# Kernel tuning notes

Measured on AMD Instinct MI355X. Metric: run time of the kernel, lower is better.

## Reference

```python
import jax, jax.numpy as jnp
import numpy as np

N_HEADS = 4  # top-k experts per token (init arg n_heads)


def setup_inputs() -> dict:
    key = jax.random.key(0)
    k1, k2, k3, k4 = jax.random.split(key, 4)
    dmodel, n_experts, expert_size = 1024, 64, 128
    B, S = 4, 2048
    x = jax.random.normal(k1, (B, S, dmodel), dtype=jnp.float32)
    # init stds follow the module: sel ~ d^-0.5, keys ~ d^-0.5, values ~ (n_experts*expert_size)^-0.5
    expert_sel = jax.random.normal(k2, (n_experts, dmodel), dtype=jnp.float32) * (dmodel ** -0.5)
    keys = jax.random.normal(k3, (n_experts, dmodel, expert_size), dtype=jnp.float32) * (dmodel ** -0.5)
    values = jax.random.normal(k4, (n_experts, expert_size, dmodel), dtype=jnp.float32) * ((n_experts * expert_size) ** -0.5)
    return {"x": x, "expert_sel": expert_sel, "keys": keys, "values": values}


def reference(x, expert_sel, keys, values):
    B, S, d = x.shape
    n_experts = keys.shape[0]
    xf = x.reshape(-1, d)                               # [N, d]
    N = xf.shape[0]
    # expert selection: sigmoid gates, top-k experts per token
    logits = xf @ expert_sel.T                           # [N, K]
    sel = jax.nn.sigmoid(logits)
    sel_val, sel_idx = jax.lax.top_k(sel, N_HEADS)       # [N, H]
    # dense gate mask: gate[n,k] = sigmoid gate if expert k selected else 0
    gates = jnp.zeros((N, n_experts), dtype=x.dtype)
    gates = gates.at[jnp.arange(N)[:, None], sel_idx].set(sel_val)
    # per-expert key projection + ReLU + gate (relu(0)*0 == 0 so dense-masked form is exact)
    h = jnp.einsum('nd,kde->nke', xf, keys)              # [N, K, E]
    scores = jax.nn.relu(h) * gates[:, :, None]
    # weighted gather-sum over per-expert values (embedding_bag mode='sum')
    out = jnp.einsum('nke,kev->nv', scores, values)      # [N, v_dim]
    return out.reshape(B, S, -1)
```

## Files before the change

### kernel.cpp

```cpp
#include <hip/hip_runtime.h>

typedef __bf16 bf16x8 __attribute__((ext_vector_type(8)));
typedef float f32x4 __attribute__((ext_vector_type(4)));

#define N_TOK 8192
#define DMODEL 1024
#define NEXP 64
#define ESIZE 128
#define WL_MAX 576
#define PREP_SPLIT 2064

__device__ __forceinline__ unsigned short f2bf(float f) {
  unsigned int u = __builtin_bit_cast(unsigned int, f);
  u += 0x7FFFu + ((u >> 16) & 1u);
  return (unsigned short)(u >> 16);
}

__device__ __forceinline__ float b2f(unsigned short u) {
  unsigned int v = ((unsigned int)u) << 16;
  return __builtin_bit_cast(float, v);
}

__device__ __forceinline__ void gld16(unsigned short* lds, const unsigned short* g) {
  __builtin_amdgcn_global_load_lds(
      (const __attribute__((address_space(1))) unsigned int*)g,
      (__attribute__((address_space(3))) unsigned int*)lds, 16, 0, 0);
}

__global__ void k_prep(const float* __restrict__ x, unsigned short* __restrict__ xh,
                       unsigned short* __restrict__ xl, const float* __restrict__ esel,
                       unsigned short* __restrict__ sh_, unsigned short* __restrict__ sl_,
                       int* __restrict__ zeroPtr) {
  int bid = blockIdx.x, tid = threadIdx.x;
  if (bid == 0 && tid < 128) zeroPtr[tid] = 0;
  size_t gid = (size_t)bid * 256 + tid;
  const size_t NX = (size_t)N_TOK * DMODEL / 16;
  const float* in;
  unsigned short *ho, *lo2;
  size_t i;
  if (gid < NX) {
    in = x; ho = xh; lo2 = xl; i = gid * 16;
  } else {
    in = esel; ho = sh_; lo2 = sl_; i = (gid - NX) * 16;
  }
#pragma unroll
  for (int c = 0; c < 2; ++c) {
    size_t ii = i + c * 8;
    float4 a = *reinterpret_cast<const float4*>(in + ii);
    float4 b = *reinterpret_cast<const float4*>(in + ii + 4);
    unsigned short h[8], l[8];
    float v[8] = {a.x, a.y, a.z, a.w, b.x, b.y, b.z, b.w};
#pragma unroll
    for (int q = 0; q < 8; ++q) {
      h[q] = f2bf(v[q]);
      l[q] = f2bf(v[q] - b2f(h[q]));
    }
    uint4 oh, ol;
    oh.x = h[0] | ((unsigned)h[1] << 16); oh.y = h[2] | ((unsigned)h[3] << 16);
    oh.z = h[4] | ((unsigned)h[5] << 16); oh.w = h[6] | ((unsigned)h[7] << 16);
    ol.x = l[0] | ((unsigned)l[1] << 16); ol.y = l[2] | ((unsigned)l[3] << 16);
    ol.z = l[4] | ((unsigned)l[5] << 16); ol.w = l[6] | ((unsigned)l[7] << 16);
    *reinterpret_cast<uint4*>(ho + ii) = oh;
    *reinterpret_cast<uint4*>(lo2 + ii) = ol;
  }
}

__global__ __launch_bounds__(512) void k_rlogit(const unsigned short* __restrict__ xh,
                                                const unsigned short* __restrict__ xl,
                                                const unsigned short* __restrict__ sh,
                                                const unsigned short* __restrict__ sl,
                                                const float* __restrict__ keys,
                                                unsigned short* __restrict__ kout,
                                                const float* __restrict__ values,
                                                unsigned short* __restrict__ vout,
                                                int4* __restrict__ idx4,
                                                float4* __restrict__ g4,
                                                int* __restrict__ gcount,
                                                int* __restrict__ glist) {
  int tid = threadIdx.x, lane = tid & 63;

  __shared__ alignas(16) unsigned short stage[24576];

  if (blockIdx.x >= 256) {
    int tt = (blockIdx.x - 256) * 2 + (tid >> 8);
    int ts = tid & 255;
    float* tb = (float*)stage + (tid >> 8) * (64 * 65);
    const float* in;
    unsigned short* out;
    int R, C;
    if (tt < 2048) { in = keys; out = kout; R = DMODEL; C = ESIZE; }
    else { in = values; out = vout; R = ESIZE; C = DMODEL; tt -= 2048; }
    int b = tt >> 5, tile = tt & 31;
    int tilesC = C >> 6;
    int tr = tile / tilesC, tc = tile % tilesC;
    const float* ip = in + (size_t)b * R * C + (size_t)tr * 64 * C + tc * 64;
    unsigned short* op = out + (size_t)b * R * C + (size_t)tc * 64 * R + tr * 64;

    int lr = ts >> 4, lc4 = (ts & 15) * 4;
#pragma unroll
    for (int p = 0; p < 4; ++p) {
      int row = p * 16 + lr;
      *reinterpret_cast<float4*>(&tb[row * 65 + lc4]) =
          *reinterpret_cast<const float4*>(ip + (size_t)row * C + lc4);
    }
    __syncthreads();
    int orow = ts >> 3, oc = (ts & 7) * 8;
#pragma unroll
    for (int p = 0; p < 2; ++p) {
      int row = p * 32 + orow;
      unsigned short h[8];
#pragma unroll
      for (int j = 0; j < 8; ++j) h[j] = f2bf(tb[(oc + j) * 65 + row]);
      uint4 ov;
      ov.x = h[0] | ((unsigned)h[1] << 16); ov.y = h[2] | ((unsigned)h[3] << 16);
      ov.z = h[4] | ((unsigned)h[5] << 16); ov.w = h[6] | ((unsigned)h[7] << 16);
      *reinterpret_cast<uint4*>(op + (size_t)row * R + oc) = ov;
    }
    return;
  }

  int tok0 = blockIdx.x * 32;
  int wv = tid >> 6, wr = wv >> 2, wc = wv & 3;
  int cc = lane & 15, grp = lane >> 4;

  int aslot = tid & 255;
  int arow = aslot >> 3, ach = aslot & 7;
  const unsigned short* srcA = (tid < 256 ? xh : xl) +
      (size_t)(tok0 + arow) * DMODEL + ((ach ^ (arow & 7)) * 8);
  int brow = tid >> 3, bch = tid & 7;
  int bsw = (bch ^ (brow & 7)) * 8;
  const unsigned short* srcBh = sh + (size_t)brow * DMODEL + bsw;
  const unsigned short* srcBl = sl + (size_t)brow * DMODEL + bsw;

  auto stg = [&](int bo , int kk) {
    unsigned short* s = stage + bo;
    gld16(s + tid * 8, srcA + kk);
    gld16(s + 4096 + tid * 8, srcBh + kk);
    gld16(s + 8192 + tid * 8, srcBl + kk);
  };

  f32x4 acc = {};
  stg(0, 0);
  __syncthreads();
  const char* sb = (const char*)stage;
  int ra = wr * 16 + cc;
  int rb = wc * 16 + cc;
  for (int t = 0; t < 16; ++t) {
    int curB = (t & 1) * 24576;
    if (t < 15) stg(((t + 1) & 1) * 12288, (t + 1) * 64);
#pragma unroll
    for (int ks = 0; ks < 2; ++ks) {
      int o_a = (((ks * 4 + grp) ^ (ra & 7)) * 16);
      int o_b = (((ks * 4 + grp) ^ (rb & 7)) * 16);
      bf16x8 aH = *reinterpret_cast<const bf16x8*>(sb + curB + ra * 128 + o_a);
      bf16x8 aL = *reinterpret_cast<const bf16x8*>(sb + curB + 4096 + ra * 128 + o_a);
      bf16x8 bH = *reinterpret_cast<const bf16x8*>(sb + curB + 8192 + rb * 128 + o_b);
      bf16x8 bL = *reinterpret_cast<const bf16x8*>(sb + curB + 16384 + rb * 128 + o_b);
      acc = __builtin_amdgcn_mfma_f32_16x16x32_bf16(aH, bH, acc, 0, 0, 0);
      acc = __builtin_amdgcn_mfma_f32_16x16x32_bf16(aH, bL, acc, 0, 0, 0);
      acc = __builtin_amdgcn_mfma_f32_16x16x32_bf16(aL, bH, acc, 0, 0, 0);
    }
    __syncthreads();
  }

  float* lg = (float*)stage;
#pragma unroll
  for (int r = 0; r < 4; ++r)
    lg[(wr * 16 + grp * 4 + r) * 68 + wc * 16 + cc] = acc[r];
  __syncthreads();

  if (tid < 32) {
    float bv0 = -3e38f, bv1 = -3e38f, bv2 = -3e38f, bv3 = -3e38f, bv4 = -3e38f;
    int bi0 = 0, bi1 = 0, bi2 = 0, bi3 = 0;
    for (int e = 0; e < 64; ++e) {
      float v = lg[tid * 68 + e];
      if (v > bv4) {
        if (v > bv0) {
          bv4 = bv3; bv3 = bv2; bi3 = bi2; bv2 = bv1; bi2 = bi1; bv1 = bv0; bi1 = bi0; bv0 = v; bi0 = e;
        } else if (v > bv1) {
          bv4 = bv3; bv3 = bv2; bi3 = bi2; bv2 = bv1; bi2 = bi1; bv1 = v; bi1 = e;
        } else if (v > bv2) {
          bv4 = bv3; bv3 = bv2; bi3 = bi2; bv2 = v; bi2 = e;
        } else if (v > bv3) {
          bv4 = bv3; bv3 = v; bi3 = e;
        } else {
          bv4 = v;
        }
      }
    }
    idx4[tok0 + tid] = make_int4(bi0, bi1, bi2, bi3);
    float4 g;
    g.x = 1.0f / (1.0f + __expf(-bv0));
    g.y = 1.0f / (1.0f + __expf(-bv1));
    g.z = 1.0f / (1.0f + __expf(-bv2));
    g.w = 1.0f / (1.0f + __expf(-bv3));
    g4[tok0 + tid] = g;
    if (bv3 - bv4 < 1e-4f) {
      int p = atomicAdd(gcount, 1);
      glist[p] = tok0 + tid;
    }
  }
}

__global__ __launch_bounds__(256) void k_refine(const float* __restrict__ x,
                                                const float* __restrict__ esel,
                                                const int* __restrict__ gcount,
                                                const int* __restrict__ glist,
                                                int4* __restrict__ idx4,
                                                float4* __restrict__ g4) {
  __shared__ double lp[256];
  __shared__ double lgt[64];
  int cnt = *gcount;
  for (int i = blockIdx.x; i < cnt; i += 64) {
    int n = glist[i];
    int e = threadIdx.x & 63, jq = threadIdx.x >> 6;
    const float* xr = x + (size_t)n * DMODEL + jq * 256;
    const float* er = esel + (size_t)e * DMODEL + jq * 256;
    double s = 0.0;
    for (int j = 0; j < 256; ++j)
      s += (double)xr[j] * (double)er[j];
    lp[threadIdx.x] = s;
    __syncthreads();
    if (threadIdx.x < 64)
      lgt[threadIdx.x] =
          lp[threadIdx.x] + lp[64 + threadIdx.x] + lp[128 + threadIdx.x] + lp[192 + threadIdx.x];
    __syncthreads();
    if (threadIdx.x == 0) {
      double bv0 = -1.0e300, bv1 = -1.0e300, bv2 = -1.0e300, bv3 = -1.0e300;
      int bi0 = 0, bi1 = 0, bi2 = 0, bi3 = 0;
      for (int e2 = 0; e2 < 64; ++e2) {
        double v = lgt[e2];
        if (v > bv3) {
          if (v > bv0) {
            bv3 = bv2; bi3 = bi2; bv2 = bv1; bi2 = bi1; bv1 = bv0; bi1 = bi0; bv0 = v; bi0 = e2;
          } else if (v > bv1) {
            bv3 = bv2; bi3 = bi2; bv2 = bv1; bi2 = bi1; bv1 = v; bi1 = e2;
          } else if (v > bv2) {
            bv3 = bv2; bi3 = bi2; bv2 = v; bi2 = e2;
          } else {
            bv3 = v; bi3 = e2;
          }
        }
      }
      idx4[n] = make_int4(bi0, bi1, bi2, bi3);
      float4 g;
      g.x = 1.0f / (1.0f + __expf(-(float)bv0));
      g.y = 1.0f / (1.0f + __expf(-(float)bv1));
      g.z = 1.0f / (1.0f + __expf(-(float)bv2));
      g.w = 1.0f / (1.0f + __expf(-(float)bv3));
      g4[n] = g;
    }
    __syncthreads();
  }
}

__global__ __launch_bounds__(256) void k_bucket(const int4* __restrict__ idx4,
                                                const float4* __restrict__ g4,
                                                int* __restrict__ btok,
                                                float* __restrict__ bgate,
                                                int* __restrict__ cnt) {
  __shared__ int lcnt[64];
  __shared__ int lbase[64];
  int tid = threadIdx.x;
  if (tid < 64) lcnt[tid] = 0;
  __syncthreads();
  int n = blockIdx.x * 256 + tid;
  int4 I = idx4[n];
  float4 G = g4[n];
  int e[4] = {I.x, I.y, I.z, I.w};
  float g[4] = {G.x, G.y, G.z, G.w};
  int pos[4];
#pragma unroll
  for (int h = 0; h < 4; ++h) pos[h] = atomicAdd(&lcnt[e[h]], 1);
  __syncthreads();
  if (tid < 64 && lcnt[tid] > 0) lbase[tid] = atomicAdd(&cnt[tid], lcnt[tid]);
  __syncthreads();
#pragma unroll
  for (int h = 0; h < 4; ++h) {
    int slot = lbase[e[h]] + pos[h];
    btok[e[h] * N_TOK + slot] = h * N_TOK + n;
    bgate[e[h] * N_TOK + slot] = g[h];
  }
}

__global__ void k_worklist(const int* __restrict__ cnt, int* __restrict__ wl) {
  int lane = threadIdx.x;
  int nt = (cnt[lane] + 63) >> 6;
  int off = nt;
  for (int d = 1; d < 64; d <<= 1) {
    int o = __shfl_up(off, d);
    if (lane >= d) off += o;
  }
  int total = __shfl(off, 63);
  off -= nt;
  for (int t = 0; t < nt; ++t) wl[off + t] = (lane << 8) | t;
  for (int i = total + lane; i < WL_MAX; i += 64) wl[i] = -1;
}

__global__ __launch_bounds__(512, 6) void k_expert(
    const unsigned short* __restrict__ xbf, const unsigned short* __restrict__ kbf,
    const unsigned short* __restrict__ vbf, const int* __restrict__ wl,
    const int* __restrict__ btok, const float* __restrict__ bgate,
    const int* __restrict__ cnt, unsigned short* __restrict__ part) {
  int wid = (blockIdx.x & 7) * (WL_MAX / 8) + (blockIdx.x >> 3);
  int wle = wl[wid];
  if (wle < 0) return;
  int k = wle >> 8, tile = wle & 255;
  int ck = cnt[k];
  int tid = threadIdx.x, lane = tid & 63;
  int wv = tid >> 6, wr = wv >> 2, wc = wv & 3;
  int cc = lane & 15, grp = lane >> 4;

  __shared__ alignas(16) unsigned short stage[25088];
  __shared__ int sRow[64];
  __shared__ float sGate[64];

  if (tid < 64) {
    int i = tile * 64 + tid;
    bool valid = i < ck;
    sRow[tid] = valid ? btok[k * N_TOK + i] : 4 * N_TOK + wid;
    sGate[tid] = valid ? bgate[k * N_TOK + i] : 0.0f;
  }
  __syncthreads();

  const unsigned short* kb = kbf + (size_t)k * (ESIZE * DMODEL);
  const unsigned short* vb = vbf + (size_t)k * (DMODEL * ESIZE);
  char* sbase = (char*)stage;

  int arow = tid >> 3, ach = tid & 7;
  const unsigned short* srcA =
      xbf + (size_t)(sRow[arow] & (N_TOK - 1)) * DMODEL + ((ach ^ (arow & 7)) * 8);
  int b1row = 64 + arow;
  const unsigned short* srcB0 = kb + (size_t)arow * DMODEL + ((ach ^ (arow & 7)) * 8);
  const unsigned short* srcB1 = kb + (size_t)b1row * DMODEL + ((ach ^ (b1row & 7)) * 8);

  auto stg1 = [&](int boB, int kk) {
    unsigned short* s = (unsigned short*)(sbase + boB);
    gld16(s + tid * 8, srcA + kk);
    gld16(s + 4096 + tid * 8, srcB0 + kk);
    gld16(s + 8192 + tid * 8, srcB1 + kk);
  };

  f32x4 acc[2][2] = {};
  stg1(0, 0);
  __syncthreads();
  for (int t = 0; t < 16; ++t) {
    int curB = (t & 1) * 24576;
    if (t < 15) stg1(((t + 1) & 1) * 24576, (t + 1) * 64);
    bf16x8 aF[2][2], bF[2][2];
#pragma unroll
    for (int ks = 0; ks < 2; ++ks) {
#pragma unroll
      for (int m = 0; m < 2; ++m) {
        int r = wr * 32 + m * 16 + cc;
        aF[ks][m] = *reinterpret_cast<const bf16x8*>(
            sbase + curB + r * 128 + (((ks * 4 + grp) ^ (r & 7)) * 16));
      }
#pragma unroll
      for (int n = 0; n < 2; ++n) {
        int r = wc * 32 + n * 16 + cc;
        bF[ks][n] = *reinterpret_cast<const bf16x8*>(
            sbase + curB + 8192 + r * 128 + (((ks * 4 + grp) ^ (r & 7)) * 16));
      }
    }
#pragma unroll
    for (int ks = 0; ks < 2; ++ks)
#pragma unroll
      for (int m = 0; m < 2; ++m)
#pragma unroll
        for (int n = 0; n < 2; ++n)
          acc[m][n] = __builtin_amdgcn_mfma_f32_16x16x32_bf16(aF[ks][m], bF[ks][n], acc[m][n], 0, 0, 0);
    __syncthreads();
  }

  int v0row = tid >> 4, vch = tid & 15;
  int v1row = 32 + v0row;
  const unsigned short* srcV0 = vb + (size_t)v0row * ESIZE + ((vch ^ (v0row & 15)) * 8);
  const unsigned short* srcV1 = vb + (size_t)v1row * ESIZE + ((vch ^ (v1row & 15)) * 8);
  auto stgV = [&](int boB, int ch) {
    unsigned short* s = (unsigned short*)(sbase + boB);
    const size_t co = (size_t)ch * 64 * ESIZE;
    gld16(s + tid * 8, srcV0 + co);
    gld16(s + 4096 + tid * 8, srcV1 + co);
  };

  stgV(17408, 0);

#pragma unroll
  for (int m = 0; m < 2; ++m) {
    int trow = wr * 32 + m * 16 + grp * 4;
#pragma unroll
    for (int n = 0; n < 2; ++n) {
      int e = wc * 32 + n * 16 + cc;
#pragma unroll
      for (int r = 0; r < 4; ++r) {
        float s = acc[m][n][r];
        s = s > 0.0f ? s * sGate[trow + r] : 0.0f;
        stage[(trow + r) * 136 + e] = f2bf(s);
      }
    }
  }
  __syncthreads();

  bf16x8 sF[2][4];
#pragma unroll
  for (int m = 0; m < 2; ++m) {
    int r = wr * 32 + m * 16 + cc;
#pragma unroll
    for (int ks = 0; ks < 4; ++ks)
      sF[m][ks] = *reinterpret_cast<const bf16x8*>((const char*)stage + r * 272 + ks * 64 + grp * 16);
  }
  unsigned short* rB[2][4];
#pragma unroll
  for (int m = 0; m < 2; ++m)
#pragma unroll
    for (int r = 0; r < 4; ++r)
      rB[m][r] = part + (size_t)sRow[wr * 32 + m * 16 + grp * 4 + r] * DMODEL + wc * 16 + cc;

  for (int ch = 0; ch < 16; ++ch) {
    int curB = 17408 + (ch & 1) * 16384;
    if (ch < 15) stgV(17408 + (((ch + 1) & 1) * 16384), ch + 1);
    int r = wc * 16 + cc;
    bf16x8 vF[4];
#pragma unroll
    for (int ks = 0; ks < 4; ++ks)
      vF[ks] = *reinterpret_cast<const bf16x8*>(
          sbase + curB + r * 256 + (((ks * 4 + grp) ^ cc) * 16));
    f32x4 o[2] = {};
#pragma unroll
    for (int ks = 0; ks < 4; ++ks)
#pragma unroll
      for (int m = 0; m < 2; ++m)
        o[m] = __builtin_amdgcn_mfma_f32_16x16x32_bf16(sF[m][ks], vF[ks], o[m], 0, 0, 0);
#pragma unroll
    for (int m = 0; m < 2; ++m)
#pragma unroll
      for (int r2 = 0; r2 < 4; ++r2)
        rB[m][r2][ch * 64] = f2bf(o[m][r2]);
    __syncthreads();
  }
}

__global__ void k_sum(const unsigned short* __restrict__ part, float* __restrict__ out) {
  size_t i = ((size_t)blockIdx.x * 256 + threadIdx.x) * 8;
  const size_t stride = (size_t)N_TOK * DMODEL;
  uint4 a = *reinterpret_cast<const uint4*>(part + i);
  uint4 b = *reinterpret_cast<const uint4*>(part + stride + i);
  uint4 c = *reinterpret_cast<const uint4*>(part + 2 * stride + i);
  uint4 d = *reinterpret_cast<const uint4*>(part + 3 * stride + i);
  float o[8];
#pragma unroll
  for (int q = 0; q < 4; ++q) {
    unsigned ua = (&a.x)[q], ub = (&b.x)[q], uc = (&c.x)[q], ud = (&d.x)[q];
    o[q * 2 + 0] = b2f((unsigned short)ua) + b2f((unsigned short)ub) +
                   b2f((unsigned short)uc) + b2f((unsigned short)ud);
    o[q * 2 + 1] = b2f((unsigned short)(ua >> 16)) + b2f((unsigned short)(ub >> 16)) +
                   b2f((unsigned short)(uc >> 16)) + b2f((unsigned short)(ud >> 16));
  }
  *reinterpret_cast<float4*>(out + i) = make_float4(o[0], o[1], o[2], o[3]);
  *reinterpret_cast<float4*>(out + i + 4) = make_float4(o[4], o[5], o[6], o[7]);
}

extern "C" void kernel_launch(void* const* d_in, const int* in_sizes, int n_in,
                              void* d_out, int out_size, void* d_ws, size_t ws_size,
                              hipStream_t stream) {
  const float* x = (const float*)d_in[0];
  const float* esel = (const float*)d_in[1];
  const float* keys = (const float*)d_in[2];
  const float* values = (const float*)d_in[3];
  float* out = (float*)d_out;

  char* p = (char*)d_ws;
  unsigned short* xbf = (unsigned short*)p; p += (size_t)N_TOK * DMODEL * 2;
  unsigned short* xlo = (unsigned short*)p; p += (size_t)N_TOK * DMODEL * 2;
  unsigned short* kbf = (unsigned short*)p; p += (size_t)NEXP * DMODEL * ESIZE * 2;
  unsigned short* vbf = (unsigned short*)p; p += (size_t)NEXP * DMODEL * ESIZE * 2;
  unsigned short* selbh = (unsigned short*)p; p += (size_t)NEXP * DMODEL * 2;
  unsigned short* selbl = (unsigned short*)p; p += (size_t)NEXP * DMODEL * 2;
  float4* g4 = (float4*)p; p += (size_t)N_TOK * 16;
  int4* idx4 = (int4*)p; p += (size_t)N_TOK * 16;
  int* btok = (int*)p; p += (size_t)NEXP * N_TOK * 4;
  float* bgate = (float*)p; p += (size_t)NEXP * N_TOK * 4;
  unsigned short* part = (unsigned short*)p;
  p += ((size_t)4 * N_TOK + WL_MAX) * DMODEL * 2;
  int* cnt = (int*)p; p += 256;
  int* gcount = (int*)p; p += 256;
  int* wl = (int*)p; p += WL_MAX * 4;
  int* glist = (int*)p; p += N_TOK * 4;
  (void)ws_size; (void)in_sizes; (void)n_in;

  k_prep<<<PREP_SPLIT, 256, 0, stream>>>(x, xbf, xlo, esel, selbh, selbl, cnt);
  k_rlogit<<<256 + 2048, 512, 0, stream>>>(xbf, xlo, selbh, selbl, keys, kbf,
                                           values, vbf, idx4, g4, gcount, glist);
  k_refine<<<64, 256, 0, stream>>>(x, esel, gcount, glist, idx4, g4);
  k_bucket<<<32, 256, 0, stream>>>(idx4, g4, btok, bgate, cnt);
  k_worklist<<<1, 64, 0, stream>>>(cnt, wl);
  k_expert<<<WL_MAX, 512, 0, stream>>>(xbf, kbf, vbf, wl, btok, bgate, cnt, part);
  k_sum<<<(N_TOK * DMODEL / 8) / 256, 256, 0, stream>>>(part, out);
}
```

Baseline: 130.2 us.

## Fold refine into bucket and compute worklist inside expert kernel

```diff
diff --git a/kernel.cpp b/kernel.cpp
--- a/kernel.cpp
+++ b/kernel.cpp
@@ -75,8 +75,7 @@
                                                 unsigned short* __restrict__ vout,
                                                 int4* __restrict__ idx4,
                                                 float4* __restrict__ g4,
-                                                int* __restrict__ gcount,
-                                                int* __restrict__ glist) {
+                                                int* __restrict__ flags) {
   int tid = threadIdx.x, lane = tid & 63;
 
   __shared__ alignas(16) unsigned short stage[24576];
@@ -195,37 +194,49 @@
     g.z = 1.0f / (1.0f + __expf(-bv2));
     g.w = 1.0f / (1.0f + __expf(-bv3));
     g4[tok0 + tid] = g;
-    if (bv3 - bv4 < 1e-4f) {
-      int p = atomicAdd(gcount, 1);
-      glist[p] = tok0 + tid;
-    }
-  }
-}
-
-__global__ __launch_bounds__(256) void k_refine(const float* __restrict__ x,
+    flags[tok0 + tid] = (bv3 - bv4 < 1e-4f) ? 1 : 0;
+  }
+}
+
+__global__ __launch_bounds__(256) void k_bucket(int4* __restrict__ idx4,
+                                                float4* __restrict__ g4,
+                                                const float* __restrict__ x,
                                                 const float* __restrict__ esel,
-                                                const int* __restrict__ gcount,
-                                                const int* __restrict__ glist,
-                                                int4* __restrict__ idx4,
-                                                float4* __restrict__ g4) {
+                                                const int* __restrict__ flags,
+                                                int* __restrict__ btok,
+                                                float* __restrict__ bgate,
+                                                int* __restrict__ cnt) {
+  __shared__ int lcnt[64];
+  __shared__ int lbase[64];
+  __shared__ int flist[256];
+  __shared__ int fnum;
   __shared__ double lp[256];
   __shared__ double lgt[64];
-  int cnt = *gcount;
-  for (int i = blockIdx.x; i < cnt; i += 64) {
-    int n = glist[i];
-    int e = threadIdx.x & 63, jq = threadIdx.x >> 6;
-    const float* xr = x + (size_t)n * DMODEL + jq * 256;
+  int tid = threadIdx.x;
+  int n = blockIdx.x * 256 + tid;
+  if (tid == 0) fnum = 0;
+  if (tid < 64) lcnt[tid] = 0;
+  __syncthreads();
+  if (flags[n]) {
+    int p = atomicAdd(&fnum, 1);
+    flist[p] = n;
+  }
+  __syncthreads();
+  int nf = fnum;
+  for (int f = 0; f < nf; ++f) {
+    int nn = flist[f];
+    int e = tid & 63, jq = tid >> 6;
+    const float* xr = x + (size_t)nn * DMODEL + jq * 256;
     const float* er = esel + (size_t)e * DMODEL + jq * 256;
     double s = 0.0;
     for (int j = 0; j < 256; ++j)
       s += (double)xr[j] * (double)er[j];
-    lp[threadIdx.x] = s;
-    __syncthreads();
-    if (threadIdx.x < 64)
-      lgt[threadIdx.x] =
-          lp[threadIdx.x] + lp[64 + threadIdx.x] + lp[128 + threadIdx.x] + lp[192 + threadIdx.x];
-    __syncthreads();
-    if (threadIdx.x == 0) {
+    lp[tid] = s;
+    __syncthreads();
+    if (tid < 64)
+      lgt[tid] = lp[tid] + lp[64 + tid] + lp[128 + tid] + lp[192 + tid];
+    __syncthreads();
+    if (tid == 0) {
       double bv0 = -1.0e300, bv1 = -1.0e300, bv2 = -1.0e300, bv3 = -1.0e300;
       int bi0 = 0, bi1 = 0, bi2 = 0, bi3 = 0;
       for (int e2 = 0; e2 < 64; ++e2) {
@@ -242,29 +253,17 @@
           }
         }
       }
-      idx4[n] = make_int4(bi0, bi1, bi2, bi3);
+      idx4[nn] = make_int4(bi0, bi1, bi2, bi3);
       float4 g;
       g.x = 1.0f / (1.0f + __expf(-(float)bv0));
       g.y = 1.0f / (1.0f + __expf(-(float)bv1));
       g.z = 1.0f / (1.0f + __expf(-(float)bv2));
       g.w = 1.0f / (1.0f + __expf(-(float)bv3));
-      g4[n] = g;
-    }
-    __syncthreads();
-  }
-}
-
-__global__ __launch_bounds__(256) void k_bucket(const int4* __restrict__ idx4,
-                                                const float4* __restrict__ g4,
-                                                int* __restrict__ btok,
-                                                float* __restrict__ bgate,
-                                                int* __restrict__ cnt) {
-  __shared__ int lcnt[64];
-  __shared__ int lbase[64];
-  int tid = threadIdx.x;
-  if (tid < 64) lcnt[tid] = 0;
-  __syncthreads();
-  int n = blockIdx.x * 256 + tid;
+      g4[nn] = g;
+    }
+    __syncthreads();
+  }
+
   int4 I = idx4[n];
   float4 G = g4[n];
   int e[4] = {I.x, I.y, I.z, I.w};
@@ -283,37 +282,39 @@
   }
 }
 
-__global__ void k_worklist(const int* __restrict__ cnt, int* __restrict__ wl) {
-  int lane = threadIdx.x;
-  int nt = (cnt[lane] + 63) >> 6;
-  int off = nt;
-  for (int d = 1; d < 64; d <<= 1) {
-    int o = __shfl_up(off, d);
-    if (lane >= d) off += o;
-  }
-  int total = __shfl(off, 63);
-  off -= nt;
-  for (int t = 0; t < nt; ++t) wl[off + t] = (lane << 8) | t;
-  for (int i = total + lane; i < WL_MAX; i += 64) wl[i] = -1;
-}
-
 __global__ __launch_bounds__(512, 6) void k_expert(
     const unsigned short* __restrict__ xbf, const unsigned short* __restrict__ kbf,
-    const unsigned short* __restrict__ vbf, const int* __restrict__ wl,
-    const int* __restrict__ btok, const float* __restrict__ bgate,
-    const int* __restrict__ cnt, unsigned short* __restrict__ part) {
+    const unsigned short* __restrict__ vbf, const int* __restrict__ btok,
+    const float* __restrict__ bgate, const int* __restrict__ cnt,
+    unsigned short* __restrict__ part) {
   int wid = (blockIdx.x & 7) * (WL_MAX / 8) + (blockIdx.x >> 3);
-  int wle = wl[wid];
-  if (wle < 0) return;
-  int k = wle >> 8, tile = wle & 255;
-  int ck = cnt[k];
   int tid = threadIdx.x, lane = tid & 63;
-  int wv = tid >> 6, wr = wv >> 2, wc = wv & 3;
-  int cc = lane & 15, grp = lane >> 4;
 
   __shared__ alignas(16) unsigned short stage[25088];
   __shared__ int sRow[64];
   __shared__ float sGate[64];
+  __shared__ int s_kt;
+
+  if (tid == 0) s_kt = -1;
+  if (tid < 64) {
+    int nt_ = (cnt[tid] + 63) >> 6;
+    int off = nt_;
+#pragma unroll
+    for (int d = 1; d < 64; d <<= 1) {
+      int o = __shfl_up(off, d);
+      if (lane >= d) off += o;
+    }
+    int lo = off - nt_;
+    if (wid >= lo && wid < off) s_kt = (tid << 8) | (wid - lo);
+  }
+  __syncthreads();
+  int kt = s_kt;
+  if (kt < 0) return;
+  int k = kt >> 8, tile = kt & 255;
+  int ck = cnt[k];
+
+  int wv = tid >> 6, wr = wv >> 2, wc = wv & 3;
+  int cc = lane & 15, grp = lane >> 4;
 
   if (tid < 64) {
     int i = tile * 64 + tid;
@@ -483,18 +484,14 @@
   float* bgate = (float*)p; p += (size_t)NEXP * N_TOK * 4;
   unsigned short* part = (unsigned short*)p;
   p += ((size_t)4 * N_TOK + WL_MAX) * DMODEL * 2;
-  int* cnt = (int*)p; p += 256;
-  int* gcount = (int*)p; p += 256;
-  int* wl = (int*)p; p += WL_MAX * 4;
-  int* glist = (int*)p; p += N_TOK * 4;
+  int* cnt = (int*)p; p += 512;
+  int* flags = (int*)p; p += N_TOK * 4;
   (void)ws_size; (void)in_sizes; (void)n_in;
 
   k_prep<<<PREP_SPLIT, 256, 0, stream>>>(x, xbf, xlo, esel, selbh, selbl, cnt);
   k_rlogit<<<256 + 2048, 512, 0, stream>>>(xbf, xlo, selbh, selbl, keys, kbf,
-                                           values, vbf, idx4, g4, gcount, glist);
-  k_refine<<<64, 256, 0, stream>>>(x, esel, gcount, glist, idx4, g4);
-  k_bucket<<<32, 256, 0, stream>>>(idx4, g4, btok, bgate, cnt);
-  k_worklist<<<1, 64, 0, stream>>>(cnt, wl);
-  k_expert<<<WL_MAX, 512, 0, stream>>>(xbf, kbf, vbf, wl, btok, bgate, cnt, part);
+                                           values, vbf, idx4, g4, flags);
+  k_bucket<<<32, 256, 0, stream>>>(idx4, g4, x, esel, flags, btok, bgate, cnt);
+  k_expert<<<WL_MAX, 512, 0, stream>>>(xbf, kbf, vbf, btok, bgate, cnt, part);
   k_sum<<<(N_TOK * DMODEL / 8) / 256, 256, 0, stream>>>(part, out);
 }
```

Measured after the change: 140.8 us. +8.2%, slower.
